# Optimization experiments

Hardware: AMD Instinct MI355X
Metric: run time of the kernel (lower is better)

## Reference

```python
import jax, jax.numpy as jnp
import numpy as np
from jax import lax

ACT_BITS = 8
O, C, K = 256, 128, 3
STRIDE, PAD = 1, 1


def setup_inputs() -> dict:
    key = jax.random.key(0)
    kx, kw = jax.random.split(key)
    x = jax.random.uniform(kx, (16, C, 56, 56), dtype=jnp.float32)
    weight = jax.random.normal(kw, (O, C, K, K), dtype=jnp.float32)
    wrange = 2 ** 8  # weight_bits
    qw = jnp.clip(jnp.round(weight * (wrange - 1)), 0, wrange - 1)
    # PCILT: pcilt[o,c,kh,kw,i] = qw[o,c,kh,kw] * i  for i in [0, 2^act_bits)
    A = 2 ** ACT_BITS
    pcilt = qw[..., None] * jnp.arange(A, dtype=jnp.float32)  # [O,C,K,K,A]
    bias = jnp.zeros((O,), dtype=jnp.float32)
    return {"x": x, "pcilt": pcilt, "bias": bias}


def reference(x, pcilt, bias):
    A = pcilt.shape[-1]
    # quantize activations to integer LUT indices in [0, A-1]
    xq = jnp.clip(jnp.round(x * (A - 1)), 0.0, A - 1.0)
    # The gather-and-sum  out[b,o,h,w] = sum_{c,kh,kw} pcilt[o,c,kh,kw, idx]
    # is mathematically identical to a conv with qw = pcilt[...,1] applied to the
    # (float-cast) quantized indices, since pcilt[...,i] == qw * i exactly.
    qw = pcilt[..., 1]  # [O,C,K,K] quantized weights
    out = lax.conv_general_dilated(
        xq, qw,
        window_strides=(STRIDE, STRIDE),
        padding=((PAD, PAD), (PAD, PAD)),
        dimension_numbers=("NCHW", "OIHW", "NCHW"),
    )
    return out + bias[None, :, None, None]
```

## Files before the change

### kernel.cpp

```cpp
#include <hip/hip_runtime.h>
#include <stdint.h>

typedef unsigned char u8;
typedef unsigned short u16;
typedef int i32x4 __attribute__((ext_vector_type(4)));
typedef u8 u8x4 __attribute__((ext_vector_type(4)));

#define B_N   16
#define C_CH  128
#define O_CH  256
#define HW    56
#define PH    58
#define PW    72

#define GLOBAL_AS __attribute__((address_space(1)))
#define LDS_AS    __attribute__((address_space(3)))

__device__ __forceinline__ void glds16(const void* g, void* l) {
    __builtin_amdgcn_global_load_lds((const GLOBAL_AS void*)g, (LDS_AS void*)l, 16, 0, 0);
}

#define XQ_OFF   0
#define BW_OFF   8552448
#define TC_OFF   (BW_OFF + 294912)
#define SA_OFF   (TC_OFF + 267264)
#define WS_OFF   (SA_OFF + 229376)

__global__ __launch_bounds__(256) void quant_pad(const float* __restrict__ x,
                                                 u8* __restrict__ xq,
                                                 int* __restrict__ Tc,
                                                 int* __restrict__ Wsum) {
    __shared__ u16 Lt[C_CH][57];
    const int hp = blockIdx.x;
    const int b = blockIdx.y;
    const int tid = threadIdx.x;
    const int h = hp - 1;
    const bool interior = (unsigned)h < HW;

    if (hp == 0 && b == 0 && tid < 256) Wsum[tid] = 0;

    if (interior) {
        const float* xr = x + ((size_t)b * C_CH * HW + h) * HW;
        for (int i = 0; i < 7; ++i) {
            int u = i * 256 + tid;
            int c = u / 14, w4 = u % 14;
            float4 v = *(const float4*)(xr + (size_t)c * (HW * HW) + w4 * 4);
            Lt[c][w4 * 4 + 0] = (u16)(int)fminf(fmaxf(rintf(v.x * 255.0f), 0.0f), 255.0f);
            Lt[c][w4 * 4 + 1] = (u16)(int)fminf(fmaxf(rintf(v.y * 255.0f), 0.0f), 255.0f);
            Lt[c][w4 * 4 + 2] = (u16)(int)fminf(fmaxf(rintf(v.z * 255.0f), 0.0f), 255.0f);
            Lt[c][w4 * 4 + 3] = (u16)(int)fminf(fmaxf(rintf(v.w * 255.0f), 0.0f), 255.0f);
        }
    }
    __syncthreads();
    u8* dst = xq + (size_t)(b * PH + hp) * 9216;
    for (int j = 0; j < 9; ++j) {
        int u = j * 256 + tid;
        int d4 = u & 3;
        int wp = (u >> 2) % PW;
        int cg = u / (4 * PW);
        int w = wp - 1;
        u8x4 v;
        if (interior && (unsigned)w < HW) {
#pragma unroll
            for (int e = 0; e < 4; ++e)
                v[e] = (u8)Lt[cg * 16 + d4 * 4 + e][w] ^ 0x80;
        } else {
            v = (u8x4){0x80, 0x80, 0x80, 0x80};
        }
        *(u8x4*)(dst + (size_t)u * 4) = v;
    }
    if (tid < PW) {
        int wp = tid, w = wp - 1;
        int s = -128 * C_CH;
        if (interior && (unsigned)w < HW) {
            for (int c = 0; c < C_CH; ++c) s += (int)Lt[c][w];
        }
        Tc[(b * PH + hp) * PW + wp] = s;
    }
}

__global__ __launch_bounds__(256) void make_w(const float* __restrict__ pcilt,
                                              u8* __restrict__ Bw,
                                              const int* __restrict__ Tc,
                                              int* __restrict__ Sa,
                                              int* __restrict__ Wsum) {
    const int bx = blockIdx.x;
    const int tid = threadIdx.x;
    if (bx < 288) {
        int v = bx * 256 + tid;
        int cb4 = v & 15;
        int o   = (v >> 4) & 255;
        int q   = (v >> 12) & 1;
        int r   = v >> 13;
        u8x4 out4;
        int part = 0;
#pragma unroll
        for (int e = 0; e < 4; ++e) {
            int c = q * 64 + cb4 * 4 + e;
            float w = pcilt[((size_t)(o * C_CH + c) * 9 + r) * 256 + 1];
            int qi = (int)w;
            out4[e] = (u8)qi ^ 0x80;
            part += qi - 128;
        }
        *(u8x4*)(Bw + (size_t)v * 4) = out4;
        part += __shfl_down(part, 1);
        part += __shfl_down(part, 2);
        part += __shfl_down(part, 4);
        part += __shfl_down(part, 8);
        if ((tid & 15) == 0) atomicAdd(&Wsum[o], part);
    } else {
        int sidx = (bx - 288) * 256 + tid;
        int w = sidx % HW;
        int h = (sidx / HW) % HW;
        int b = sidx / (HW * HW);
        const int* t = Tc + (b * PH + h) * PW + w;
        int s = 0;
#pragma unroll
        for (int dh = 0; dh < 3; ++dh)
#pragma unroll
            for (int dw = 0; dw < 3; ++dw)
                s += t[dh * PW + dw];
        Sa[(b * HW + h) * 64 + w] = s;
    }
}

__global__ __launch_bounds__(256) void conv_mfma(const u8* __restrict__ xq,
                                                 const u8* __restrict__ Bw,
                                                 const int* __restrict__ Sa,
                                                 const int* __restrict__ Wsum,
                                                 const float* __restrict__ bias,
                                                 float* __restrict__ out) {
    __shared__ __align__(16) u8 Is[4][128][16];

    const int tid = threadIdx.x;
    const int o_blk = blockIdx.x * 128;
    const int h0 = blockIdx.y * 2;
    const int b = blockIdx.z;

    const int lane = tid & 63;
    const int wid = tid >> 6;
    const int wo = wid & 1;
    const int wm = wid >> 1;
    const int quad = lane >> 4;
    const int lrow = lane & 15;

    i32x4 acc[4][4];
#pragma unroll
    for (int i = 0; i < 4; i++)
#pragma unroll
        for (int j = 0; j < 4; j++) acc[i][j] = (i32x4){0, 0, 0, 0};

    const int sdh = wid & 1;
    const int scg = (wid >> 1) * 2;
    const u8* gbase = xq + (size_t)(b * PH + h0 + sdh) * 9216 + lane * 16;
    const u8* wl = Bw + (size_t)(o_blk + wo * 64 + lrow) * 64 + quad * 16;

    for (int r = 0; r < 9; ++r) {
        const int kh = r / 3, kw = r % 3;
#pragma unroll
        for (int q = 0; q < 2; ++q) {
            const int st = r * 2 + q;
            __syncthreads();
#pragma unroll
            for (int cc = 0; cc < 2; ++cc) {
                const int cg = scg + cc;
                const u8* src = gbase + (size_t)kh * 9216 + (q * 4 + cg) * (PW * 16) + kw * 16;
                glds16(src, &Is[cg][sdh * 64][0]);
            }
            i32x4 af[4];
#pragma unroll
            for (int i = 0; i < 4; ++i)
                af[i] = *(const i32x4*)(wl + ((size_t)st * 256 + i * 16) * 64);
            __syncthreads();
            i32x4 bfr[4];
#pragma unroll
            for (int j = 0; j < 4; ++j)
                bfr[j] = *(const i32x4*)&Is[quad][wm * 64 + j * 16 + lrow][0];
#pragma unroll
            for (int i = 0; i < 4; ++i)
#pragma unroll
                for (int j = 0; j < 4; ++j)
                    acc[i][j] = __builtin_amdgcn_mfma_i32_16x16x64_i8(af[i], bfr[j], acc[i][j], 0, 0, 0);
        }
    }

    const int hh = h0 + wm;
    int sa_j[4];
#pragma unroll
    for (int j = 0; j < 4; ++j) {
        const int w = j * 16 + lrow;
        sa_j[j] = (w < HW) ? Sa[(b * HW + hh) * 64 + w] : 0;
    }
#pragma unroll
    for (int i = 0; i < 4; i++) {
        const int obase = o_blk + wo * 64 + i * 16 + quad * 4;
#pragma unroll
        for (int rg = 0; rg < 4; ++rg) {
            const int o = obase + rg;
            const int wsum = Wsum[o];
            const float bs = bias[o];
#pragma unroll
            for (int j = 0; j < 4; ++j) {
                const int w = j * 16 + lrow;
                if (w < HW) {
                    int tot = acc[i][j][rg] + 128 * (sa_j[j] + wsum) + 18874368;
                    out[(((size_t)b * O_CH + o) * HW + hh) * HW + w] = (float)tot + bs;
                }
            }
        }
    }
}

extern "C" void kernel_launch(void* const* d_in, const int* in_sizes, int n_in,
                              void* d_out, int out_size, void* d_ws, size_t ws_size,
                              hipStream_t stream) {
    const float* x     = (const float*)d_in[0];
    const float* pcilt = (const float*)d_in[1];
    const float* bias  = (const float*)d_in[2];
    float* out = (float*)d_out;

    u8* ws = (u8*)d_ws;
    u8*  xq   = ws + XQ_OFF;
    u8*  Bw   = ws + BW_OFF;
    int* Tc   = (int*)(ws + TC_OFF);
    int* Sa   = (int*)(ws + SA_OFF);
    int* Wsum = (int*)(ws + WS_OFF);

    quant_pad<<<dim3(PH, B_N), 256, 0, stream>>>(x, xq, Tc, Wsum);
    make_w<<<484, 256, 0, stream>>>(pcilt, Bw, Tc, Sa, Wsum);
    conv_mfma<<<dim3(O_CH / 128, HW / 2, B_N), dim3(256), 0, stream>>>(xq, Bw, Sa, Wsum, bias, out);
}
```

Before: 406.2 us.

## Merge quantize and weight-prep kernels, compute window sums inside conv

The activation quantize/pad kernel and the weight-packing kernel are combined into one launch with block ranges split by role. The 3x3 window sum of per-pixel channel totals moves from a separate pass into the conv kernel, which now computes it into shared memory from Tc. The Wsum zeroing moves to a hipMemsetAsync. This removes one kernel launch and the Sa round trip through global memory, at the cost of an extra memset call and some redundant Tc reads across output-channel blocks.

```diff
diff --git a/kernel.cpp b/kernel.cpp
--- a/kernel.cpp
+++ b/kernel.cpp
@@ -23,71 +23,64 @@
 #define XQ_OFF   0
 #define BW_OFF   8552448
 #define TC_OFF   (BW_OFF + 294912)
-#define SA_OFF   (TC_OFF + 267264)
-#define WS_OFF   (SA_OFF + 229376)
-
-__global__ __launch_bounds__(256) void quant_pad(const float* __restrict__ x,
-                                                 u8* __restrict__ xq,
-                                                 int* __restrict__ Tc,
-                                                 int* __restrict__ Wsum) {
-    __shared__ u16 Lt[C_CH][57];
-    const int hp = blockIdx.x;
-    const int b = blockIdx.y;
-    const int tid = threadIdx.x;
-    const int h = hp - 1;
-    const bool interior = (unsigned)h < HW;
-
-    if (hp == 0 && b == 0 && tid < 256) Wsum[tid] = 0;
-
-    if (interior) {
-        const float* xr = x + ((size_t)b * C_CH * HW + h) * HW;
-        for (int i = 0; i < 7; ++i) {
-            int u = i * 256 + tid;
-            int c = u / 14, w4 = u % 14;
-            float4 v = *(const float4*)(xr + (size_t)c * (HW * HW) + w4 * 4);
-            Lt[c][w4 * 4 + 0] = (u16)(int)fminf(fmaxf(rintf(v.x * 255.0f), 0.0f), 255.0f);
-            Lt[c][w4 * 4 + 1] = (u16)(int)fminf(fmaxf(rintf(v.y * 255.0f), 0.0f), 255.0f);
-            Lt[c][w4 * 4 + 2] = (u16)(int)fminf(fmaxf(rintf(v.z * 255.0f), 0.0f), 255.0f);
-            Lt[c][w4 * 4 + 3] = (u16)(int)fminf(fmaxf(rintf(v.w * 255.0f), 0.0f), 255.0f);
-        }
-    }
-    __syncthreads();
-    u8* dst = xq + (size_t)(b * PH + hp) * 9216;
-    for (int j = 0; j < 9; ++j) {
-        int u = j * 256 + tid;
-        int d4 = u & 3;
-        int wp = (u >> 2) % PW;
-        int cg = u / (4 * PW);
-        int w = wp - 1;
-        u8x4 v;
-        if (interior && (unsigned)w < HW) {
-#pragma unroll
-            for (int e = 0; e < 4; ++e)
-                v[e] = (u8)Lt[cg * 16 + d4 * 4 + e][w] ^ 0x80;
-        } else {
-            v = (u8x4){0x80, 0x80, 0x80, 0x80};
-        }
-        *(u8x4*)(dst + (size_t)u * 4) = v;
-    }
-    if (tid < PW) {
-        int wp = tid, w = wp - 1;
-        int s = -128 * C_CH;
-        if (interior && (unsigned)w < HW) {
-            for (int c = 0; c < C_CH; ++c) s += (int)Lt[c][w];
-        }
-        Tc[(b * PH + hp) * PW + wp] = s;
-    }
-}
-
-__global__ __launch_bounds__(256) void make_w(const float* __restrict__ pcilt,
-                                              u8* __restrict__ Bw,
-                                              const int* __restrict__ Tc,
-                                              int* __restrict__ Sa,
-                                              int* __restrict__ Wsum) {
+#define WS_OFF   (TC_OFF + 267264)
+
+__global__ __launch_bounds__(256) void prep(const float* __restrict__ x,
+                                            const float* __restrict__ pcilt,
+                                            u8* __restrict__ xq,
+                                            u8* __restrict__ Bw,
+                                            int* __restrict__ Tc,
+                                            int* __restrict__ Wsum) {
     const int bx = blockIdx.x;
     const int tid = threadIdx.x;
-    if (bx < 288) {
-        int v = bx * 256 + tid;
+
+    if (bx < PH * B_N) {
+        __shared__ u16 Lt[C_CH][57];
+        const int hp = bx % PH;
+        const int b = bx / PH;
+        const int h = hp - 1;
+        const bool interior = (unsigned)h < HW;
+
+        if (interior) {
+            const float* xr = x + ((size_t)b * C_CH * HW + h) * HW;
+            for (int i = 0; i < 7; ++i) {
+                int u = i * 256 + tid;
+                int c = u / 14, w4 = u % 14;
+                float4 v = *(const float4*)(xr + (size_t)c * (HW * HW) + w4 * 4);
+                Lt[c][w4 * 4 + 0] = (u16)(int)fminf(fmaxf(rintf(v.x * 255.0f), 0.0f), 255.0f);
+                Lt[c][w4 * 4 + 1] = (u16)(int)fminf(fmaxf(rintf(v.y * 255.0f), 0.0f), 255.0f);
+                Lt[c][w4 * 4 + 2] = (u16)(int)fminf(fmaxf(rintf(v.z * 255.0f), 0.0f), 255.0f);
+                Lt[c][w4 * 4 + 3] = (u16)(int)fminf(fmaxf(rintf(v.w * 255.0f), 0.0f), 255.0f);
+            }
+        }
+        __syncthreads();
+        u8* dst = xq + (size_t)(b * PH + hp) * 9216;
+        for (int j = 0; j < 9; ++j) {
+            int u = j * 256 + tid;
+            int d4 = u & 3;
+            int wp = (u >> 2) % PW;
+            int cg = u / (4 * PW);
+            int w = wp - 1;
+            u8x4 v;
+            if (interior && (unsigned)w < HW) {
+#pragma unroll
+                for (int e = 0; e < 4; ++e)
+                    v[e] = (u8)Lt[cg * 16 + d4 * 4 + e][w] ^ 0x80;
+            } else {
+                v = (u8x4){0x80, 0x80, 0x80, 0x80};
+            }
+            *(u8x4*)(dst + (size_t)u * 4) = v;
+        }
+        if (tid < PW) {
+            int wp = tid, w = wp - 1;
+            int s = -128 * C_CH;
+            if (interior && (unsigned)w < HW) {
+                for (int c = 0; c < C_CH; ++c) s += (int)Lt[c][w];
+            }
+            Tc[(b * PH + hp) * PW + wp] = s;
+        }
+    } else {
+        int v = (bx - PH * B_N) * 256 + tid;
         int cb4 = v & 15;
         int o   = (v >> 4) & 255;
         int q   = (v >> 12) & 1;
@@ -108,29 +101,17 @@
         part += __shfl_down(part, 4);
         part += __shfl_down(part, 8);
         if ((tid & 15) == 0) atomicAdd(&Wsum[o], part);
-    } else {
-        int sidx = (bx - 288) * 256 + tid;
-        int w = sidx % HW;
-        int h = (sidx / HW) % HW;
-        int b = sidx / (HW * HW);
-        const int* t = Tc + (b * PH + h) * PW + w;
-        int s = 0;
-#pragma unroll
-        for (int dh = 0; dh < 3; ++dh)
-#pragma unroll
-            for (int dw = 0; dw < 3; ++dw)
-                s += t[dh * PW + dw];
-        Sa[(b * HW + h) * 64 + w] = s;
     }
 }
 
 __global__ __launch_bounds__(256) void conv_mfma(const u8* __restrict__ xq,
                                                  const u8* __restrict__ Bw,
-                                                 const int* __restrict__ Sa,
+                                                 const int* __restrict__ Tc,
                                                  const int* __restrict__ Wsum,
                                                  const float* __restrict__ bias,
                                                  float* __restrict__ out) {
     __shared__ __align__(16) u8 Is[4][128][16];
+    __shared__ int Sa_l[2][64];
 
     const int tid = threadIdx.x;
     const int o_blk = blockIdx.x * 128;
@@ -144,6 +125,20 @@
     const int quad = lane >> 4;
     const int lrow = lane & 15;
 
+    if (tid < 128) {
+        const int rr = tid >> 6, w = tid & 63;
+        int s = 0;
+        if (w < HW) {
+            const int* t = Tc + (b * PH + h0 + rr) * PW + w;
+#pragma unroll
+            for (int dh = 0; dh < 3; ++dh)
+#pragma unroll
+                for (int dw = 0; dw < 3; ++dw)
+                    s += t[dh * PW + dw];
+        }
+        Sa_l[rr][w] = s;
+    }
+
     i32x4 acc[4][4];
 #pragma unroll
     for (int i = 0; i < 4; i++)
@@ -189,7 +184,7 @@
 #pragma unroll
     for (int j = 0; j < 4; ++j) {
         const int w = j * 16 + lrow;
-        sa_j[j] = (w < HW) ? Sa[(b * HW + hh) * 64 + w] : 0;
+        sa_j[j] = (w < HW) ? Sa_l[wm][w] : 0;
     }
 #pragma unroll
     for (int i = 0; i < 4; i++) {
@@ -223,10 +218,9 @@
     u8*  xq   = ws + XQ_OFF;
     u8*  Bw   = ws + BW_OFF;
     int* Tc   = (int*)(ws + TC_OFF);
-    int* Sa   = (int*)(ws + SA_OFF);
     int* Wsum = (int*)(ws + WS_OFF);
 
-    quant_pad<<<dim3(PH, B_N), 256, 0, stream>>>(x, xq, Tc, Wsum);
-    make_w<<<484, 256, 0, stream>>>(pcilt, Bw, Tc, Sa, Wsum);
-    conv_mfma<<<dim3(O_CH / 128, HW / 2, B_N), dim3(256), 0, stream>>>(xq, Bw, Sa, Wsum, bias, out);
-}
+    hipMemsetAsync(Wsum, 0, O_CH * sizeof(int), stream);
+    prep<<<PH * B_N + 288, 256, 0, stream>>>(x, pcilt, xq, Bw, Tc, Wsum);
+    conv_mfma<<<dim3(O_CH / 128, HW / 2, B_N), dim3(256), 0, stream>>>(xq, Bw, Tc, Wsum, bias, out);
+}
```

After: 404.5 us. No clear change (-0.4%).
